# Optimization experiments

Hardware: AMD Instinct MI355X
Metric: run time of the kernel (lower is better)

## Reference

```python
import jax, jax.numpy as jnp
import numpy as np

B, T, D_MODEL, D_STATE = 4, 4096, 1024, 256


def setup_inputs() -> dict:
    key = jax.random.key(0)
    ks = jax.random.split(key, 6)
    return {
        "x": jax.random.normal(ks[0], (B, T, D_MODEL), dtype=jnp.float32),
        "state": jnp.zeros((B, D_STATE), dtype=jnp.float32),
        "W_in": jax.random.normal(ks[1], (D_MODEL, D_STATE), dtype=jnp.float32) / np.sqrt(D_MODEL),
        "b_in": jnp.zeros((D_STATE,), dtype=jnp.float32),
        "lambda_param": jax.random.normal(ks[2], (D_STATE,), dtype=jnp.float32),
        "gamma_param": jax.random.normal(ks[3], (D_STATE,), dtype=jnp.float32),
        "W_out": jax.random.normal(ks[4], (D_STATE, D_MODEL), dtype=jnp.float32) / np.sqrt(D_STATE),
        "b_out": jnp.zeros((D_MODEL,), dtype=jnp.float32),
    }


def reference(x, state, W_in, b_in, lambda_param, gamma_param, W_out, b_out):
    # u: [B, T, d_state]
    u = jnp.einsum("btd,ds->bts", x, W_in) + b_in
    decay = jax.nn.sigmoid(lambda_param)          # [d_state]
    gu = gamma_param * u                          # [B, T, d_state]

    # linear recurrence h_t = decay * h_{t-1} + gu_t via associative scan over T
    # elements: (a, b) representing h -> a*h + b; combine: (a2*a1, a2*b1 + b2)
    a = jnp.broadcast_to(decay, gu.shape)         # [B, T, d_state]

    def combine(l, r):
        a1, b1 = l
        a2, b2 = r
        return (a2 * a1, a2 * b1 + b2)

    A, Bc = jax.lax.associative_scan(combine, (a, gu), axis=1)
    h = A * state[:, None, :] + Bc                # [B, T, d_state]

    y = jnp.einsum("bts,sd->btd", h, W_out) + b_out
    return y, h[:, -1, :]
```

## Files before the change

### kernel.cpp

```cpp
#include <hip/hip_runtime.h>
#include <hip/hip_bf16.h>
#include <math.h>

#define BB 4
#define TT 4096
#define DM 1024
#define DS 256
#define MROWS (BB*TT)

#define LCH 32
#define NCH (TT/LCH)

#define BM 128

typedef __attribute__((ext_vector_type(8))) _Float16 half8v;
typedef __attribute__((ext_vector_type(4))) float float4v;

__device__ __forceinline__ float sigmoidf_dev(float x) {
    return 1.0f / (1.0f + expf(-x));
}

__device__ __forceinline__ void gload16(const void* g, void* l) {
    __builtin_amdgcn_global_load_lds(
        (const __attribute__((address_space(1))) void*)g,
        (__attribute__((address_space(3))) void*)l, 16, 0, 0);
}

__global__ __launch_bounds__(256) void cvt_inputs(
    const float* __restrict__ x, _Float16* __restrict__ xf,
    const float* __restrict__ W1, _Float16* __restrict__ T1,
    const float* __restrict__ W2, _Float16* __restrict__ T2)
{
    if (blockIdx.x < 8192) {
        size_t u = (size_t)blockIdx.x * 256 + threadIdx.x;
        const float* p = x + u * 8;
        float4 a = *(const float4*)p;
        float4 b = *(const float4*)(p + 4);
        half8v h;
        h[0] = (_Float16)a.x; h[1] = (_Float16)a.y; h[2] = (_Float16)a.z; h[3] = (_Float16)a.w;
        h[4] = (_Float16)b.x; h[5] = (_Float16)b.y; h[6] = (_Float16)b.z; h[7] = (_Float16)b.w;
        *(half8v*)(xf + u * 8) = h;
    } else {
        const int blk = blockIdx.x - 8192;
        const int half = blk >> 10;
        int idx = (blk & 1023) * 256 + threadIdx.x;
        const float* W = half ? W2 : W1;
        _Float16* T = half ? T2 : T1;
        const int K = half ? DS : DM;
        const int N = half ? DM : DS;
        int n = idx / K, k = idx - n * K;
        T[idx] = (_Float16)W[(size_t)k * N + n];
    }
}

__global__ __launch_bounds__(256) void gemm1_fused(
    const _Float16* __restrict__ A, const _Float16* __restrict__ Bt,
    _Float16* __restrict__ gu,
    const float* __restrict__ bias, const float* __restrict__ scale,
    const float* __restrict__ lam, float* __restrict__ csum)
{
    constexpr int K = DM;
    constexpr int BN = 64, BK = 64, NF = 2, WCOLS = 32;
    constexpr int NT = K / BK;
    constexpr int BUFB = 24576;
    __shared__ char smem[3 * BUFB];

    const int nwg = gridDim.x;
    const int bid = blockIdx.x;
    const int wgid = (bid & 7) * (nwg >> 3) + (bid >> 3);
    const int GN = DS / BN;
    const int bm = wgid / GN;
    const int bn = wgid - bm * GN;

    const int tid  = threadIdx.x;
    const int lane = tid & 63;
    const int wv   = tid >> 6;
    const int wr   = wv >> 1;
    const int wc   = wv & 1;
    const int lrow = lane & 15;
    const int q16  = lane >> 4;

    float4v acc[4][NF] = {};

#define STAGE1(T, Q)                                                              \
    do {                                                                          \
        char* base_ = smem + (Q) * BUFB;                                          \
        const int k0_ = (T) * BK;                                                 \
        _Pragma("unroll")                                                         \
        for (int p = 0; p < 4; p++) {                                             \
            int c = tid + p * 256, r = c >> 3, chp = c & 7;                       \
            const _Float16* g_ = A + (size_t)(bm * BM + r) * K + k0_              \
                                   + ((chp ^ (r & 7)) << 3);                      \
            gload16(g_, base_ + c * 16);                                          \
        }                                                                         \
        _Pragma("unroll")                                                         \
        for (int p = 0; p < 2; p++) {                                             \
            int c = tid + p * 256, r = c >> 3, chp = c & 7;                       \
            const _Float16* g_ = Bt + (size_t)(bn * BN + r) * K + k0_             \
                                    + ((chp ^ (r & 7)) << 3);                     \
            gload16(g_, base_ + 16384 + c * 16);                                  \
        }                                                                         \
    } while (0)

#define COMPUTE1(Q)                                                               \
    do {                                                                          \
        char* const rb = smem + (Q) * BUFB;                                       \
        half8v a[4][2], b[NF][2];                                                 \
        _Pragma("unroll")                                                         \
        for (int i = 0; i < 4; i++) {                                             \
            int row = wr * 64 + i * 16 + lrow;                                    \
            _Pragma("unroll")                                                     \
            for (int ss = 0; ss < 2; ss++) {                                      \
                int ch = (ss * 4 + q16) ^ (row & 7);                              \
                a[i][ss] = *(const half8v*)(rb + row * 128 + ch * 16);            \
            }                                                                     \
        }                                                                         \
        _Pragma("unroll")                                                         \
        for (int j = 0; j < NF; j++) {                                            \
            int row = wc * WCOLS + j * 16 + lrow;                                 \
            _Pragma("unroll")                                                     \
            for (int ss = 0; ss < 2; ss++) {                                      \
                int ch = (ss * 4 + q16) ^ (row & 7);                              \
                b[j][ss] = *(const half8v*)(rb + 16384 + row * 128 + ch * 16);    \
            }                                                                     \
        }                                                                         \
        _Pragma("unroll")                                                         \
        for (int ss = 0; ss < 2; ss++)                                            \
            _Pragma("unroll")                                                     \
            for (int i = 0; i < 4; i++)                                           \
                _Pragma("unroll")                                                 \
                for (int j = 0; j < NF; j++)                                      \
                    acc[i][j] = __builtin_amdgcn_mfma_f32_16x16x32_f16(           \
                        a[i][ss], b[j][ss], acc[i][j], 0, 0, 0);                  \
    } while (0)

    STAGE1(0, 0);
    STAGE1(1, 1);

    int qc = 0;
    for (int t = 0; t < NT - 1; ++t) {
        asm volatile("s_waitcnt vmcnt(6)" ::: "memory");
        __builtin_amdgcn_s_barrier();
        if (t + 2 < NT) {
            int qn = qc + 2; if (qn >= 3) qn -= 3;
            STAGE1(t + 2, qn);
        }
        COMPUTE1(qc);
        qc = (qc == 2) ? 0 : qc + 1;
    }
    asm volatile("s_waitcnt vmcnt(0)" ::: "memory");
    __builtin_amdgcn_s_barrier();
    COMPUTE1(qc);
    __syncthreads();

    float* gul = (float*)smem;
#pragma unroll
    for (int j = 0; j < NF; j++) {
        int col = bn * BN + wc * WCOLS + j * 16 + lrow;
        float bi = bias[col];
        float sc = scale[col];
#pragma unroll
        for (int i = 0; i < 4; i++) {
            int r0 = bm * BM + wr * 64 + i * 16 + q16 * 4;
#pragma unroll
            for (int reg = 0; reg < 4; reg++) {
                float v = (acc[i][j][reg] + bi) * sc;
                gu[(size_t)(r0 + reg) * DS + col] = (_Float16)v;
                int lr = wr * 64 + i * 16 + q16 * 4 + reg;
                int lc = wc * WCOLS + j * 16 + lrow;
                gul[lr * 68 + lc] = v;
            }
        }
    }

    __syncthreads();
    const int lc = tid >> 6;
    const int ch = tid & 63;
    const int gcol = bn * BN + ch;
    const float d = sigmoidf_dev(lam[gcol]);
    float h = 0.0f;
#pragma unroll
    for (int rr = 0; rr < LCH; rr++)
        h = fmaf(d, h, gul[(lc * LCH + rr) * 68 + ch]);
    const int row0 = bm * BM;
    const int b    = row0 >> 12;
    const int gch  = ((row0 & 4095) >> 5) + lc;
    csum[((size_t)b * NCH + gch) * DS + gcol] = h;
#undef STAGE1
#undef COMPUTE1
}

__global__ __launch_bounds__(256) void gemm2_f16(
    const _Float16* __restrict__ A, const _Float16* __restrict__ Bt,
    float* __restrict__ C, const float* __restrict__ bias)
{
    constexpr int BN = 128, BK = 32, NF = 4, WCOLS = 64;
    constexpr int K = DS;
    constexpr int NT = K / BK;
    constexpr int BUFB = 16384;
    __shared__ char smem[3 * BUFB];

    const int nwg = gridDim.x;
    const int bid = blockIdx.x;
    const int wgid = (bid & 7) * (nwg >> 3) + (bid >> 3);
    const int GN = DM / BN;
    const int bm = wgid / GN;
    const int bn = wgid - bm * GN;

    const int tid  = threadIdx.x;
    const int lane = tid & 63;
    const int wv   = tid >> 6;
    const int wr   = wv >> 1;
    const int wc   = wv & 1;
    const int lrow = lane & 15;
    const int q16  = lane >> 4;

    float4v acc[4][NF] = {};

#define STAGE2(T, Q)                                                              \
    do {                                                                          \
        char* base_ = smem + (Q) * BUFB;                                          \
        const int k0_ = (T) * BK;                                                 \
        _Pragma("unroll")                                                         \
        for (int p = 0; p < 2; p++) {                                             \
            int c = tid + p * 256, r = c >> 2, chp = c & 3;                       \
            const _Float16* g_ = A + (size_t)(bm * BM + r) * K + k0_              \
                                   + ((chp ^ ((r >> 1) & 3)) << 3);               \
            gload16(g_, base_ + c * 16);                                          \
        }                                                                         \
        _Pragma("unroll")                                                         \
        for (int p = 0; p < 2; p++) {                                             \
            int c = tid + p * 256, r = c >> 2, chp = c & 3;                       \
            const _Float16* g_ = Bt + (size_t)(bn * BN + r) * K + k0_             \
                                    + ((chp ^ ((r >> 1) & 3)) << 3);              \
            gload16(g_, base_ + 8192 + c * 16);                                   \
        }                                                                         \
    } while (0)

#define COMPUTE2(Q)                                                               \
    do {                                                                          \
        char* const rb = smem + (Q) * BUFB;                                       \
        half8v a[4], b[NF];                                                       \
        _Pragma("unroll")                                                         \
        for (int i = 0; i < 4; i++) {                                             \
            int row = wr * 64 + i * 16 + lrow;                                    \
            int ch = q16 ^ ((row >> 1) & 3);                                      \
            a[i] = *(const half8v*)(rb + row * 64 + ch * 16);                     \
        }                                                                         \
        _Pragma("unroll")                                                         \
        for (int j = 0; j < NF; j++) {                                            \
            int row = wc * WCOLS + j * 16 + lrow;                                 \
            int ch = q16 ^ ((row >> 1) & 3);                                      \
            b[j] = *(const half8v*)(rb + 8192 + row * 64 + ch * 16);              \
        }                                                                         \
        _Pragma("unroll")                                                         \
        for (int i = 0; i < 4; i++)                                               \
            _Pragma("unroll")                                                     \
            for (int j = 0; j < NF; j++)                                          \
                acc[i][j] = __builtin_amdgcn_mfma_f32_16x16x32_f16(               \
                    a[i], b[j], acc[i][j], 0, 0, 0);                              \
    } while (0)

    STAGE2(0, 0);
    STAGE2(1, 1);

    int qc = 0;
    for (int t = 0; t < NT - 1; ++t) {
        asm volatile("s_waitcnt vmcnt(4)" ::: "memory");
        __builtin_amdgcn_s_barrier();
        if (t + 2 < NT) {
            int qn = qc + 2; if (qn >= 3) qn -= 3;
            STAGE2(t + 2, qn);
        }
        COMPUTE2(qc);
        qc = (qc == 2) ? 0 : qc + 1;
    }
    asm volatile("s_waitcnt vmcnt(0)" ::: "memory");
    __builtin_amdgcn_s_barrier();
    COMPUTE2(qc);

#pragma unroll
    for (int j = 0; j < NF; j++) {
        int col = bn * BN + wc * WCOLS + j * 16 + lrow;
        float bi = bias[col];
#pragma unroll
        for (int i = 0; i < 4; i++) {
            int r0 = bm * BM + wr * 64 + i * 16 + q16 * 4;
#pragma unroll
            for (int reg = 0; reg < 4; reg++)
                C[(size_t)(r0 + reg) * DM + col] = acc[i][j][reg] + bi;
        }
    }
#undef STAGE2
#undef COMPUTE2
}

__global__ __launch_bounds__(256) void carry_scan(
    const float* __restrict__ csum, const float* __restrict__ state,
    const float* __restrict__ lam, float* __restrict__ carry, float* __restrict__ hlast)
{
    const int s = threadIdx.x;
    const int b = blockIdx.x;
    const float d = sigmoidf_dev(lam[s]);
    float dL = d;
#pragma unroll
    for (int i = 0; i < 5; i++) dL *= dL;
    float H = state[(size_t)b * DS + s];
#pragma unroll 8
    for (int k = 0; k < NCH; k++) {
        carry[((size_t)b * NCH + k) * DS + s] = H;
        H = fmaf(dL, H, csum[((size_t)b * NCH + k) * DS + s]);
    }
    hlast[(size_t)b * DS + s] = H;
}

__global__ __launch_bounds__(256) void scan_final(
    const _Float16* __restrict__ gu, const float* __restrict__ lam,
    const float* __restrict__ carry, _Float16* __restrict__ hf)
{
    const int s = threadIdx.x;
    const int chunk = blockIdx.x;
    const int b = blockIdx.y;
    const float d = sigmoidf_dev(lam[s]);
    const size_t base = ((size_t)b * TT + (size_t)chunk * LCH) * DS + s;
    const _Float16* p = gu + base;
    _Float16* ph = hf + base;
    float h = carry[((size_t)b * NCH + chunk) * DS + s];
#pragma unroll
    for (int t = 0; t < LCH; t++) {
        h = fmaf(d, h, (float)p[(size_t)t * DS]);
        ph[(size_t)t * DS] = (_Float16)h;
    }
}

extern "C" void kernel_launch(void* const* d_in, const int* in_sizes, int n_in,
                              void* d_out, int out_size, void* d_ws, size_t ws_size,
                              hipStream_t stream) {
    const float* x     = (const float*)d_in[0];
    const float* state = (const float*)d_in[1];
    const float* W_in  = (const float*)d_in[2];
    const float* b_in  = (const float*)d_in[3];
    const float* lam   = (const float*)d_in[4];
    const float* gamma = (const float*)d_in[5];
    const float* W_out = (const float*)d_in[6];
    const float* b_out = (const float*)d_in[7];

    float* y     = (float*)d_out;
    float* hlast = y + (size_t)MROWS * DM;

    char* ws = (char*)d_ws;
    const size_t MB = 1024 * 1024;
    _Float16*  gu    = (_Float16*)(ws);
    float*     csum  = (float*)(ws + 8 * MB);
    float*     carry = (float*)(ws + 8 * MB + 512 * 1024);
    _Float16*  hf    = (_Float16*)(ws + 9 * MB);
    _Float16*  w1t   = (_Float16*)(ws + 17 * MB);
    _Float16*  w2t   = (_Float16*)(ws + 17 * MB + 512 * 1024);
    _Float16*  xf    = (_Float16*)(ws + 18 * MB);

    cvt_inputs<<<dim3(10240), dim3(256), 0, stream>>>(x, xf, W_in, w1t, W_out, w2t);

    gemm1_fused<<<dim3((MROWS / BM) * (DS / 64)), dim3(256), 0, stream>>>(
        xf, w1t, gu, b_in, gamma, lam, csum);

    carry_scan<<<dim3(BB), dim3(256), 0, stream>>>(csum, state, lam, carry, hlast);
    scan_final<<<dim3(NCH, BB), dim3(256), 0, stream>>>(gu, lam, carry, hf);

    gemm2_f16<<<dim3((MROWS / BM) * (DM / 128)), dim3(256), 0, stream>>>(
        hf, w2t, y, b_out);
}
```

Measured before the change: 66.90 us.

## Fuse fp32-to-fp16 conversion of x into the first GEMM's A-tile loading

```diff
diff --git a/kernel.cpp b/kernel.cpp
--- a/kernel.cpp
+++ b/kernel.cpp
@@ -14,10 +14,18 @@
 #define BM 128
 
 typedef __attribute__((ext_vector_type(8))) _Float16 half8v;
+typedef __attribute__((ext_vector_type(2))) _Float16 half2v;
 typedef __attribute__((ext_vector_type(4))) float float4v;
 
 __device__ __forceinline__ float sigmoidf_dev(float x) {
     return 1.0f / (1.0f + expf(-x));
+}
+
+__device__ __forceinline__ half2v cvt2_rtz(float a, float b) {
+    auto r = __builtin_amdgcn_cvt_pkrtz(a, b);
+    union { decltype(r) i; half2v o; } cv;
+    cv.i = r;
+    return cv.o;
 }
 
 __device__ __forceinline__ void gload16(const void* g, void* l) {
@@ -26,35 +34,22 @@
         (__attribute__((address_space(3))) void*)l, 16, 0, 0);
 }
 
-__global__ __launch_bounds__(256) void cvt_inputs(
-    const float* __restrict__ x, _Float16* __restrict__ xf,
+__global__ __launch_bounds__(256) void cvt_weights(
     const float* __restrict__ W1, _Float16* __restrict__ T1,
     const float* __restrict__ W2, _Float16* __restrict__ T2)
 {
-    if (blockIdx.x < 8192) {
-        size_t u = (size_t)blockIdx.x * 256 + threadIdx.x;
-        const float* p = x + u * 8;
-        float4 a = *(const float4*)p;
-        float4 b = *(const float4*)(p + 4);
-        half8v h;
-        h[0] = (_Float16)a.x; h[1] = (_Float16)a.y; h[2] = (_Float16)a.z; h[3] = (_Float16)a.w;
-        h[4] = (_Float16)b.x; h[5] = (_Float16)b.y; h[6] = (_Float16)b.z; h[7] = (_Float16)b.w;
-        *(half8v*)(xf + u * 8) = h;
-    } else {
-        const int blk = blockIdx.x - 8192;
-        const int half = blk >> 10;
-        int idx = (blk & 1023) * 256 + threadIdx.x;
-        const float* W = half ? W2 : W1;
-        _Float16* T = half ? T2 : T1;
-        const int K = half ? DS : DM;
-        const int N = half ? DM : DS;
-        int n = idx / K, k = idx - n * K;
-        T[idx] = (_Float16)W[(size_t)k * N + n];
-    }
-}
-
-__global__ __launch_bounds__(256) void gemm1_fused(
-    const _Float16* __restrict__ A, const _Float16* __restrict__ Bt,
+    const int half = blockIdx.x >> 10;
+    int idx = (blockIdx.x & 1023) * 256 + threadIdx.x;
+    const float* W = half ? W2 : W1;
+    _Float16* T = half ? T2 : T1;
+    const int K = half ? DS : DM;
+    const int N = half ? DM : DS;
+    int n = idx / K, k = idx - n * K;
+    T[idx] = (_Float16)W[(size_t)k * N + n];
+}
+
+__global__ __launch_bounds__(256, 2) void gemm1_fused(
+    const float* __restrict__ x, const _Float16* __restrict__ Bt,
     _Float16* __restrict__ gu,
     const float* __restrict__ bias, const float* __restrict__ scale,
     const float* __restrict__ lam, float* __restrict__ csum)
@@ -80,25 +75,42 @@
     const int lrow = lane & 15;
     const int q16  = lane >> 4;
 
+    const int arow  = tid >> 1;
+    const int acolf = (tid & 1) * 32;
+    const int acb   = (tid & 1) * 4;
+
     float4v acc[4][NF] = {};
-
-#define STAGE1(T, Q)                                                              \
-    do {                                                                          \
-        char* base_ = smem + (Q) * BUFB;                                          \
-        const int k0_ = (T) * BK;                                                 \
-        _Pragma("unroll")                                                         \
-        for (int p = 0; p < 4; p++) {                                             \
-            int c = tid + p * 256, r = c >> 3, chp = c & 7;                       \
-            const _Float16* g_ = A + (size_t)(bm * BM + r) * K + k0_              \
-                                   + ((chp ^ (r & 7)) << 3);                      \
-            gload16(g_, base_ + c * 16);                                          \
-        }                                                                         \
+    float4 rA[2][8];
+
+#define LOADREG(S, T)                                                             \
+    do {                                                                          \
+        const float* g_ = x + (size_t)(bm * BM + arow) * K + (T) * BK + acolf;    \
+        _Pragma("unroll")                                                         \
+        for (int p = 0; p < 8; p++) rA[S][p] = *(const float4*)(g_ + 4 * p);      \
+    } while (0)
+
+#define WRITE_A(S, Q)                                                             \
+    do {                                                                          \
+        char* base_ = smem + (Q) * BUFB + arow * 128;                             \
+        _Pragma("unroll")                                                         \
+        for (int ci = 0; ci < 4; ci++) {                                          \
+            union { half2v h2[4]; half8v h8; } u_;                                \
+            u_.h2[0] = cvt2_rtz(rA[S][2 * ci].x,     rA[S][2 * ci].y);            \
+            u_.h2[1] = cvt2_rtz(rA[S][2 * ci].z,     rA[S][2 * ci].w);            \
+            u_.h2[2] = cvt2_rtz(rA[S][2 * ci + 1].x, rA[S][2 * ci + 1].y);        \
+            u_.h2[3] = cvt2_rtz(rA[S][2 * ci + 1].z, rA[S][2 * ci + 1].w);        \
+            *(half8v*)(base_ + (((acb + ci) ^ (arow & 7)) << 4)) = u_.h8;         \
+        }                                                                         \
+    } while (0)
+
+#define STAGE_B(T, Q)                                                             \
+    do {                                                                          \
         _Pragma("unroll")                                                         \
         for (int p = 0; p < 2; p++) {                                             \
             int c = tid + p * 256, r = c >> 3, chp = c & 7;                       \
-            const _Float16* g_ = Bt + (size_t)(bn * BN + r) * K + k0_             \
+            const _Float16* g_ = Bt + (size_t)(bn * BN + r) * K + (T) * BK        \
                                     + ((chp ^ (r & 7)) << 3);                     \
-            gload16(g_, base_ + 16384 + c * 16);                                  \
+            gload16(g_, smem + (Q) * BUFB + 16384 + c * 16);                      \
         }                                                                         \
     } while (0)
 
@@ -134,24 +146,30 @@
                         a[i][ss], b[j][ss], acc[i][j], 0, 0, 0);                  \
     } while (0)
 
-    STAGE1(0, 0);
-    STAGE1(1, 1);
-
-    int qc = 0;
-    for (int t = 0; t < NT - 1; ++t) {
-        asm volatile("s_waitcnt vmcnt(6)" ::: "memory");
+    STAGE_B(0, 0); LOADREG(0, 0);
+    STAGE_B(1, 1); LOADREG(1, 1);
+    asm volatile("s_waitcnt vmcnt(10)" ::: "memory");
+    WRITE_A(0, 0);
+    asm volatile("s_waitcnt lgkmcnt(0)" ::: "memory");
+    __builtin_amdgcn_s_barrier();
+
+#pragma unroll
+    for (int t = 0; t < NT; ++t) {
+        if (t + 2 < NT) {
+            STAGE_B(t + 2, (t + 2) % 3);
+            LOADREG(t & 1, t + 2);
+        }
+        COMPUTE1(t % 3);
+        if (t + 1 < NT) {
+            if (t + 2 < NT)
+                asm volatile("s_waitcnt vmcnt(10)" ::: "memory");
+            else
+                asm volatile("s_waitcnt vmcnt(0)" ::: "memory");
+            WRITE_A((t + 1) & 1, (t + 1) % 3);
+        }
+        asm volatile("s_waitcnt lgkmcnt(0)" ::: "memory");
         __builtin_amdgcn_s_barrier();
-        if (t + 2 < NT) {
-            int qn = qc + 2; if (qn >= 3) qn -= 3;
-            STAGE1(t + 2, qn);
-        }
-        COMPUTE1(qc);
-        qc = (qc == 2) ? 0 : qc + 1;
-    }
-    asm volatile("s_waitcnt vmcnt(0)" ::: "memory");
-    __builtin_amdgcn_s_barrier();
-    COMPUTE1(qc);
-    __syncthreads();
+    }
 
     float* gul = (float*)smem;
 #pragma unroll
@@ -186,7 +204,9 @@
     const int b    = row0 >> 12;
     const int gch  = ((row0 & 4095) >> 5) + lc;
     csum[((size_t)b * NCH + gch) * DS + gcol] = h;
-#undef STAGE1
+#undef LOADREG
+#undef WRITE_A
+#undef STAGE_B
 #undef COMPUTE1
 }
 
@@ -356,12 +376,11 @@
     _Float16*  hf    = (_Float16*)(ws + 9 * MB);
     _Float16*  w1t   = (_Float16*)(ws + 17 * MB);
     _Float16*  w2t   = (_Float16*)(ws + 17 * MB + 512 * 1024);
-    _Float16*  xf    = (_Float16*)(ws + 18 * MB);
-
-    cvt_inputs<<<dim3(10240), dim3(256), 0, stream>>>(x, xf, W_in, w1t, W_out, w2t);
+
+    cvt_weights<<<dim3(2048), dim3(256), 0, stream>>>(W_in, w1t, W_out, w2t);
 
     gemm1_fused<<<dim3((MROWS / BM) * (DS / 64)), dim3(256), 0, stream>>>(
-        xf, w1t, gu, b_in, gamma, lam, csum);
+        x, w1t, gu, b_in, gamma, lam, csum);
 
     carry_scan<<<dim3(BB), dim3(256), 0, stream>>>(csum, state, lam, carry, hlast);
     scan_final<<<dim3(NCH, BB), dim3(256), 0, stream>>>(gu, lam, carry, hf);
```

Result: slower. 78.99 us (+18.1%).

## Deepen gemm1 pipeline to five stages with smaller K tiles

Applied to the files above, without the earlier changes.

```diff
diff --git a/kernel.cpp b/kernel.cpp
--- a/kernel.cpp
+++ b/kernel.cpp
@@ -60,10 +60,10 @@
     const float* __restrict__ lam, float* __restrict__ csum)
 {
     constexpr int K = DM;
-    constexpr int BN = 64, BK = 64, NF = 2, WCOLS = 32;
+    constexpr int BN = 64, BK = 32, NF = 2, WCOLS = 32;
     constexpr int NT = K / BK;
-    constexpr int BUFB = 24576;
-    __shared__ char smem[3 * BUFB];
+    constexpr int BUFB = 12288;
+    __shared__ char smem[5 * BUFB];
 
     const int nwg = gridDim.x;
     const int bid = blockIdx.x;
@@ -87,70 +87,57 @@
         char* base_ = smem + (Q) * BUFB;                                          \
         const int k0_ = (T) * BK;                                                 \
         _Pragma("unroll")                                                         \
-        for (int p = 0; p < 4; p++) {                                             \
-            int c = tid + p * 256, r = c >> 3, chp = c & 7;                       \
+        for (int p = 0; p < 2; p++) {                                             \
+            int c = tid + p * 256, r = c >> 2, chp = c & 3;                       \
             const _Float16* g_ = A + (size_t)(bm * BM + r) * K + k0_              \
-                                   + ((chp ^ (r & 7)) << 3);                      \
+                                   + ((chp ^ ((r >> 1) & 3)) << 3);               \
             gload16(g_, base_ + c * 16);                                          \
         }                                                                         \
-        _Pragma("unroll")                                                         \
-        for (int p = 0; p < 2; p++) {                                             \
-            int c = tid + p * 256, r = c >> 3, chp = c & 7;                       \
+        {                                                                         \
+            int c = tid, r = c >> 2, chp = c & 3;                                 \
             const _Float16* g_ = Bt + (size_t)(bn * BN + r) * K + k0_             \
-                                    + ((chp ^ (r & 7)) << 3);                     \
-            gload16(g_, base_ + 16384 + c * 16);                                  \
+                                    + ((chp ^ ((r >> 1) & 3)) << 3);              \
+            gload16(g_, base_ + 8192 + c * 16);                                   \
         }                                                                         \
     } while (0)
 
 #define COMPUTE1(Q)                                                               \
     do {                                                                          \
         char* const rb = smem + (Q) * BUFB;                                       \
-        half8v a[4][2], b[NF][2];                                                 \
+        half8v a[4], b[NF];                                                       \
         _Pragma("unroll")                                                         \
         for (int i = 0; i < 4; i++) {                                             \
             int row = wr * 64 + i * 16 + lrow;                                    \
-            _Pragma("unroll")                                                     \
-            for (int ss = 0; ss < 2; ss++) {                                      \
-                int ch = (ss * 4 + q16) ^ (row & 7);                              \
-                a[i][ss] = *(const half8v*)(rb + row * 128 + ch * 16);            \
-            }                                                                     \
+            int ch = q16 ^ ((row >> 1) & 3);                                      \
+            a[i] = *(const half8v*)(rb + row * 64 + ch * 16);                     \
         }                                                                         \
         _Pragma("unroll")                                                         \
         for (int j = 0; j < NF; j++) {                                            \
             int row = wc * WCOLS + j * 16 + lrow;                                 \
+            int ch = q16 ^ ((row >> 1) & 3);                                      \
+            b[j] = *(const half8v*)(rb + 8192 + row * 64 + ch * 16);              \
+        }                                                                         \
+        _Pragma("unroll")                                                         \
+        for (int i = 0; i < 4; i++)                                               \
             _Pragma("unroll")                                                     \
-            for (int ss = 0; ss < 2; ss++) {                                      \
-                int ch = (ss * 4 + q16) ^ (row & 7);                              \
-                b[j][ss] = *(const half8v*)(rb + 16384 + row * 128 + ch * 16);    \
-            }                                                                     \
-        }                                                                         \
-        _Pragma("unroll")                                                         \
-        for (int ss = 0; ss < 2; ss++)                                            \
-            _Pragma("unroll")                                                     \
-            for (int i = 0; i < 4; i++)                                           \
-                _Pragma("unroll")                                                 \
-                for (int j = 0; j < NF; j++)                                      \
-                    acc[i][j] = __builtin_amdgcn_mfma_f32_16x16x32_f16(           \
-                        a[i][ss], b[j][ss], acc[i][j], 0, 0, 0);                  \
+            for (int j = 0; j < NF; j++)                                          \
+                acc[i][j] = __builtin_amdgcn_mfma_f32_16x16x32_f16(               \
+                    a[i], b[j], acc[i][j], 0, 0, 0);                              \
     } while (0)
 
-    STAGE1(0, 0);
-    STAGE1(1, 1);
-
-    int qc = 0;
-    for (int t = 0; t < NT - 1; ++t) {
-        asm volatile("s_waitcnt vmcnt(6)" ::: "memory");
+    STAGE1(0, 0); STAGE1(1, 1); STAGE1(2, 2); STAGE1(3, 3);
+
+#pragma unroll
+    for (int t = 0; t < NT; ++t) {
+        const int rem = NT - 1 - t;
+        if (rem >= 3)      asm volatile("s_waitcnt vmcnt(9)" ::: "memory");
+        else if (rem == 2) asm volatile("s_waitcnt vmcnt(6)" ::: "memory");
+        else if (rem == 1) asm volatile("s_waitcnt vmcnt(3)" ::: "memory");
+        else               asm volatile("s_waitcnt vmcnt(0)" ::: "memory");
         __builtin_amdgcn_s_barrier();
-        if (t + 2 < NT) {
-            int qn = qc + 2; if (qn >= 3) qn -= 3;
-            STAGE1(t + 2, qn);
-        }
-        COMPUTE1(qc);
-        qc = (qc == 2) ? 0 : qc + 1;
-    }
-    asm volatile("s_waitcnt vmcnt(0)" ::: "memory");
-    __builtin_amdgcn_s_barrier();
-    COMPUTE1(qc);
+        if (t + 4 < NT) STAGE1(t + 4, (t + 4) % 5);
+        COMPUTE1(t % 5);
+    }
     __syncthreads();
 
     float* gul = (float*)smem;
```

After: 67.72 us. No clear change (+1.2%).
